# Kernel tuning notes

Measured on AMD Instinct MI355X. Metric: run time of the kernel, lower is better.

## Reference

```python
import jax, jax.numpy as jnp
from jax import lax
import numpy as np

NE = 8          # ne_num
IDX_REF = 4     # ne_num // 2
EPS_BN = 1e-5


def conv2d(x, w, b=None, pad=0):
    out = lax.conv_general_dilated(x, w, (1, 1), [(pad, pad), (pad, pad)],
                                   dimension_numbers=('NCHW', 'OIHW', 'NCHW'))
    if b is not None:
        out = out + b[None, :, None, None]
    return out


def bn(x, gamma, beta):
    # training-mode batch norm (biased variance), as nn.BatchNorm2d in train()
    mu = x.mean(axis=(0, 2, 3), keepdims=True)
    var = x.var(axis=(0, 2, 3), keepdims=True)
    xn = (x - mu) * lax.rsqrt(var + EPS_BN)
    return xn * gamma[None, :, None, None] + beta[None, :, None, None]


def gauss_win(sigma):
    # sigma: (B,1). window_size=3 -> bias = [-1, 0, -1]; pop center of 3x3 -> (B,8)
    bias = jnp.array([-1.0, 0.0, -1.0], dtype=sigma.dtype)
    g = jnp.exp(bias[None, :] / (2.0 * sigma ** 2))            # (B,3)
    w1 = g / g.sum(axis=1, keepdims=True)                      # (B,3)
    w2 = (w1[:, :, None] * w1[:, None, :]).reshape(-1, 9)      # (B,9)
    return jnp.concatenate([w2[:, :4], w2[:, 5:]], axis=1)     # (B,8) center removed


def bilinear(img, y, x):
    # img: (B,H,W); y,x: (B,K,H,W) float sample coords; zero padding outside
    B, H, W = img.shape
    y0 = jnp.floor(y); x0 = jnp.floor(x)
    wy1 = y - y0; wy0 = 1.0 - wy1
    wx1 = x - x0; wx0 = 1.0 - wx1
    imgf = img.reshape(B, -1)

    def gather(yi, xi):
        yii = yi.astype(jnp.int32); xii = xi.astype(jnp.int32)
        valid = (yii >= 0) & (yii < H) & (xii >= 0) & (xii < W)
        idx = jnp.clip(yii, 0, H - 1) * W + jnp.clip(xii, 0, W - 1)
        v = jnp.take_along_axis(imgf, idx.reshape(B, -1), axis=1).reshape(idx.shape)
        return jnp.where(valid, v, 0.0)

    return (wy0 * wx0 * gather(y0, x0) + wy0 * wx1 * gather(y0, x0 + 1.0)
            + wy1 * wx0 * gather(y0 + 1.0, x0) + wy1 * wx1 * gather(y0 + 1.0, x0 + 1.0))


def modulated_deform_conv_1x9(fusion, offset, mask):
    # ModulatedDeformConvFunction with weight=ones(1,1,3,3), bias=0, stride=1,
    # pad=1, dilation=1, groups=1, deformable_groups=1.
    # fusion: (B,1,H,W); offset: (B,9,2,H,W) [per-neighbor (dy,dx)]; mask: (B,9,H,W)
    B, _, H, W = fusion.shape
    k = jnp.arange(9)
    py = (k // 3 - 1).astype(fusion.dtype)[None, :, None, None]
    px = (k % 3 - 1).astype(fusion.dtype)[None, :, None, None]
    hh = jnp.arange(H, dtype=fusion.dtype)[None, None, :, None]
    ww = jnp.arange(W, dtype=fusion.dtype)[None, None, None, :]
    y = hh + py + offset[:, :, 0]
    x = ww + px + offset[:, :, 1]
    samp = bilinear(fusion[:, 0], y, x)            # (B,9,H,W)
    return (mask * samp).sum(axis=1, keepdims=True)  # (B,1,H,W)


def _forward(feat, g1_w, g1_g, g1_b, g2_w, g2_g, g2_b, g3_w, g3_bias,
             f1_w, f1_g, f1_b, f2_w, f2_bias,
             s1_w, s1_b, s2_w, s2_b, s3_w, s3_b,
             oa1_w, oa1_g, oa1_b, oa2_w, oa2_g, oa2_b, oa3_w, oa3_bias,
             aff_scale):
    B, _, H, W = feat.shape
    # guid branch (5x5 convs)
    guid = jax.nn.relu(bn(conv2d(feat, g1_w, pad=2), g1_g, g1_b))
    guid = jax.nn.relu(bn(conv2d(guid, g2_w, pad=2), g2_g, g2_b))
    guid = conv2d(guid, g3_w, g3_bias, pad=2)                      # (B,8,H,W)
    # fuse branch
    f = jax.nn.relu(bn(conv2d(feat, f1_w, pad=1), f1_g, f1_b))
    fusion = jnp.tanh(conv2d(f, f2_w, f2_bias, pad=1))             # (B,1,H,W)
    # sigma branch (CAM, detached input)
    fd = lax.stop_gradient(feat)
    p = fd.mean(axis=(2, 3))                                       # (B,32)
    h = jax.nn.celu(p @ s1_w.T + s1_b)
    h = jax.nn.celu(h @ s2_w.T + s2_b)
    sigma = jax.nn.relu(h @ s3_w.T + s3_b) + 0.001                 # (B,1)
    # get_off_aff(guid, sigma, sigma_gamma=0.2, window_size=3)
    oa = jax.nn.relu(bn(conv2d(guid, oa1_w, pad=2), oa1_g, oa1_b))
    oa = jax.nn.relu(bn(conv2d(oa, oa2_w, pad=2), oa2_g, oa2_b))
    oa = conv2d(oa, oa3_w, oa3_bias, pad=2)                        # (B,24,H,W)
    o1, o2, affc = jnp.split(oa, 3, axis=1)                        # each (B,8,H,W)
    off = jnp.concatenate([o1, o2], axis=1).reshape(B, NE, 2, H, W)
    zero_ref = jnp.zeros((B, 1, 2, H, W), dtype=off.dtype)
    offset = jnp.concatenate([off[:, :IDX_REF], zero_ref, off[:, IDX_REF:]], axis=1)  # (B,9,2,H,W)
    gk = gauss_win(sigma + 0.2)                                    # (B,8)
    aff = jnp.tanh(affc) / (aff_scale + 1e-5) + gk[:, :, None, None]
    sa = jnp.abs(aff).sum(axis=1, keepdims=True) + 1e-5
    sa = jnp.maximum(sa, 1.0)
    aff = aff / sa
    aff_ref = 1.0 - aff.sum(axis=1, keepdims=True)
    aff9 = jnp.concatenate([aff[:, :IDX_REF], aff_ref, aff[:, IDX_REF:]], axis=1)  # (B,9,H,W)
    # gauss_filter (times=1) + abs
    gfusion = jnp.abs(modulated_deform_conv_1x9(fusion, offset, aff9))
    return gfusion


def setup_inputs() -> dict:
    key = jax.random.key(0)
    ks = list(jax.random.split(key, 32))
    B, C, H, W = 8, 32, 320, 320
    ne = NE
    d = {}
    d['feat'] = jax.random.normal(ks[0], (B, C, H, W), jnp.float32)

    def wconv(k, o, i, s):
        return jax.random.normal(k, (o, i, s, s), jnp.float32) * (1.0 / np.sqrt(i * s * s))

    def wlin(k, o, i):
        return jax.random.normal(k, (o, i), jnp.float32) * (1.0 / np.sqrt(i))

    # guid: 32->32 (5), 32->8 (5), 8->8 (5, bias)
    d['g1_w'] = wconv(ks[1], C, C, 5); d['g1_g'] = jnp.ones(C) + 0.1 * jax.random.normal(ks[2], (C,)); d['g1_b'] = 0.1 * jax.random.normal(ks[3], (C,))
    d['g2_w'] = wconv(ks[4], ne, C, 5); d['g2_g'] = jnp.ones(ne) + 0.1 * jax.random.normal(ks[5], (ne,)); d['g2_b'] = 0.1 * jax.random.normal(ks[6], (ne,))
    d['g3_w'] = wconv(ks[7], ne, ne, 5); d['g3_bias'] = 0.1 * jax.random.normal(ks[8], (ne,))
    # fuse: 32->32 (3), 32->1 (3, bias)
    d['f1_w'] = wconv(ks[9], C, C, 3); d['f1_g'] = jnp.ones(C) + 0.1 * jax.random.normal(ks[10], (C,)); d['f1_b'] = 0.1 * jax.random.normal(ks[11], (C,))
    d['f2_w'] = wconv(ks[12], 1, C, 3); d['f2_bias'] = 0.1 * jax.random.normal(ks[13], (1,))
    # gen_sigma CAM: 32->16->16->1
    d['s1_w'] = wlin(ks[14], 16, C); d['s1_b'] = 0.1 * jax.random.normal(ks[15], (16,))
    d['s2_w'] = wlin(ks[16], 16, 16); d['s2_b'] = 0.1 * jax.random.normal(ks[17], (16,))
    d['s3_w'] = wlin(ks[18], 1, 16); d['s3_b'] = 0.1 * jax.random.normal(ks[19], (1,))
    # conv_off_aff: 8->8 (5), 8->24 (5), 24->24 (5, bias)
    d['oa1_w'] = wconv(ks[20], ne, ne, 5); d['oa1_g'] = jnp.ones(ne) + 0.1 * jax.random.normal(ks[21], (ne,)); d['oa1_b'] = 0.1 * jax.random.normal(ks[22], (ne,))
    d['oa2_w'] = wconv(ks[23], 3 * ne, ne, 5); d['oa2_g'] = jnp.ones(3 * ne) + 0.1 * jax.random.normal(ks[24], (3 * ne,)); d['oa2_b'] = 0.1 * jax.random.normal(ks[25], (3 * ne,))
    d['oa3_w'] = wconv(ks[26], 3 * ne, 3 * ne, 5); d['oa3_bias'] = 0.1 * jax.random.normal(ks[27], (3 * ne,))
    # aff_scale_const = aff_gamma * ne_num = 0.5 * 8
    d['aff_scale'] = jnp.full((1,), 4.0, jnp.float32)
    return d


def reference(feat, g1_w, g1_g, g1_b, g2_w, g2_g, g2_b, g3_w, g3_bias,
              f1_w, f1_g, f1_b, f2_w, f2_bias,
              s1_w, s1_b, s2_w, s2_b, s3_w, s3_b,
              oa1_w, oa1_g, oa1_b, oa2_w, oa2_g, oa2_b, oa3_w, oa3_bias,
              aff_scale):
    return _forward(feat, g1_w, g1_g, g1_b, g2_w, g2_g, g2_b, g3_w, g3_bias,
                    f1_w, f1_g, f1_b, f2_w, f2_bias,
                    s1_w, s1_b, s2_w, s2_b, s3_w, s3_b,
                    oa1_w, oa1_g, oa1_b, oa2_w, oa2_g, oa2_b, oa3_w, oa3_bias,
                    aff_scale)
```

## Files before the change

kernel.cpp:

```cpp
#include <hip/hip_runtime.h>
#include <hip/hip_bf16.h>
#include <math.h>

#define B_   8
#define H_   320
#define W_   320
#define HW_  (320*320)

typedef __attribute__((ext_vector_type(8))) short bf16x8;
typedef __attribute__((ext_vector_type(4))) short bf16x4s;
typedef __attribute__((ext_vector_type(4))) float f32x4;

__device__ __forceinline__ short f2b(float v){
    __hip_bfloat16 h = __float2bfloat16(v);
    return *(short*)&h;
}
__device__ __forceinline__ float bf2f(short v){
    unsigned u = ((unsigned)(unsigned short)v) << 16;
    return __uint_as_float(u);
}

__global__ void convert_k(const float* __restrict__ in, short* __restrict__ out,
                          float* __restrict__ psum){
    const int b  = blockIdx.y;
    const int px = blockIdx.x*256 + threadIdx.x;
    const float* src = in + (long)b*32*HW_ + px;
    short* dst = out + ((long)b*HW_ + px)*32;
    float f[32];
    short v[32];
    #pragma unroll
    for (int c=0;c<32;++c){ f[c] = src[(long)c*HW_]; v[c] = f2b(f[c]); }
    #pragma unroll
    for (int s=0;s<4;++s)
        *(bf16x8*)(dst + s*8) = *(bf16x8*)(v + s*8);
    #pragma unroll
    for (int c=0;c<32;++c){
        float s = f[c];
        #pragma unroll
        for (int o=1;o<64;o<<=1) s += __shfl_xor(s, o, 64);
        f[c] = s;
    }
    __shared__ float red[4][32];
    const int lane = threadIdx.x & 63, wid = threadIdx.x >> 6;
    if (lane < 32) red[wid][lane] = f[lane];
    __syncthreads();
    if (threadIdx.x < 32)
        atomicAdd(&psum[b*32 + threadIdx.x],
                  red[0][threadIdx.x]+red[1][threadIdx.x]+red[2][threadIdx.x]+red[3][threadIdx.x]);
}

__global__ void repack_k(const float* __restrict__ sf1, const float* __restrict__ sf2,
                         const float* __restrict__ sg1, const float* __restrict__ sg2,
                         const float* __restrict__ sg3, const float* __restrict__ so1,
                         const float* __restrict__ so2, const float* __restrict__ so3,
                         short* __restrict__ dst){
    const int cum[8]  = {9216,13824,39424,52224,55808,59392,66560,92160};
    const int CINs[8] = {32,32,32,32, 8, 8, 8,24};
    const int CIps[8] = {32,32,32,32, 8, 8, 8,32};
    const int COUTs[8]= {32, 1,32, 8, 8, 8,24,24};
    const int MTs[8]  = { 2, 1, 2, 1, 1, 1, 2, 2};
    const int Ks[8]   = { 3, 3, 5, 5, 5, 5, 5, 5};
    int i = blockIdx.x*256 + threadIdx.x;
    if (i >= 92160) return;
    int s = 0;
    while (i >= cum[s]) ++s;
    const int base = s ? cum[s-1] : 0;
    const int il = i - base;
    const float* src = (s==0)?sf1:(s==1)?sf2:(s==2)?sg1:(s==3)?sg2:(s==4)?sg3:(s==5)?so1:(s==6)?so2:so3;
    const int kl   = il & 31;
    const int co_l = (il >> 5) & 15;
    const int rem  = il >> 9;
    const int MT = MTs[s];
    const int mt = rem % MT;
    const int c  = rem / MT;
    const int K = Ks[s];
    int tap, ci;
    if (CIps[s] == 32){ tap = (c % K)*K + (c / K); ci = kl; }
    else              { tap = c*4 + (kl>>3); ci = kl & 7; }
    const int co = mt*16 + co_l;
    float v = 0.f;
    if (co < COUTs[s] && ci < CINs[s] && tap < K*K){
        const int ky = tap / K, kx = tap - ky*K;
        v = src[((co*CINs[s] + ci)*K + ky)*K + kx];
    }
    dst[i] = f2b(v);
}

__device__ __forceinline__
float deform_px(const float* val, const float* __restrict__ fus_b,
                const float* __restrict__ gk_b, float inv_s, int y, int x){
    float aff[8]; float sa = 0.f;
    #pragma unroll
    for (int n=0;n<8;++n){
        float a = tanhf(val[16+n]) * inv_s + gk_b[n];
        aff[n] = a; sa += fabsf(a);
    }
    sa += 1e-5f;
    sa = fmaxf(sa, 1.f);
    const float isa = 1.f/sa;
    float ssum = 0.f;
    #pragma unroll
    for (int n=0;n<8;++n){ aff[n] *= isa; ssum += aff[n]; }
    const float aff_ref = 1.f - ssum;

    float o = 0.f;
    #pragma unroll
    for (int k=0;k<9;++k){
        float dy, dx, m;
        if (k == 4){ dy = 0.f; dx = 0.f; m = aff_ref; }
        else {
            const int n = (k < 4) ? k : k-1;
            dy = val[2*n];
            dx = val[2*n+1];
            m  = aff[n];
        }
        float yy = (float)(y + k/3 - 1) + dy;
        float xx = (float)(x + k%3 - 1) + dx;
        float y0f = floorf(yy), x0f = floorf(xx);
        int   y0 = (int)y0f,    x0i = (int)x0f;
        float wy1 = yy - y0f, wy0 = 1.f - wy1;
        float wx1 = xx - x0f, wx0 = 1.f - wx1;
        float v00 = (y0  >=0 && y0  <H_ && x0i  >=0 && x0i  <W_) ? fus_b[ y0   *W_ + x0i  ] : 0.f;
        float v01 = (y0  >=0 && y0  <H_ && x0i+1>=0 && x0i+1<W_) ? fus_b[ y0   *W_ + x0i+1] : 0.f;
        float v10 = (y0+1>=0 && y0+1<H_ && x0i  >=0 && x0i  <W_) ? fus_b[(y0+1)*W_ + x0i  ] : 0.f;
        float v11 = (y0+1>=0 && y0+1<H_ && x0i+1>=0 && x0i+1<W_) ? fus_b[(y0+1)*W_ + x0i+1] : 0.f;
        o += m * (wy0*(wx0*v00 + wx1*v01) + wy1*(wx0*v10 + wx1*v11));
    }
    return fabsf(o);
}

template<int CIN, int CIp, int COUT, int MT, int K,
         bool IN_BN, bool OUT_STATS, int OUT_MODE, int OCP>
__global__ __launch_bounds__(256, 4)
void mconv_k(const void* __restrict__ inv,
             const float* __restrict__ bn_sum, const float* __restrict__ bn_sq,
             const float* __restrict__ gamma, const float* __restrict__ beta,
             const short* __restrict__ wr, const float* __restrict__ bias,
             void* __restrict__ outv,
             float* __restrict__ osum, float* __restrict__ osq,
             const float* __restrict__ fus, const float* __restrict__ gk,
             const float* __restrict__ aff_scale){
    constexpr int PAD = K/2;
    constexpr int TH  = 8;
    constexpr int LW  = 32 + K - 1;
    constexpr int LH  = TH + K - 1;
    constexpr int STR = (CIp==32) ? 40 : 8;
    constexpr int NTAPS  = K*K;
    constexpr int NCHUNK = (CIp==32) ? NTAPS : (NTAPS*CIp + 31)/32;
    constexpr int INB  = LH*LW*STR*2;
    constexpr int DUMPB = 256*33*4;
    constexpr int LDSB = (OUT_MODE==3 && INB < DUMPB) ? DUMPB : INB;

    __shared__ __align__(16) char ldsraw[LDSB];
    short* lds_in = (short*)ldsraw;
    __shared__ float sc_sh[2][32];
    __shared__ float red[2][4][32];

    const int tid = threadIdx.x;
    const int b   = blockIdx.z;
    const int x0  = blockIdx.x*32, y0 = blockIdx.y*TH;

    if (IN_BN){
        if (tid < 32){
            float s = 1.f, sh2 = 0.f;
            if (tid < CIN){
                const float invN = 1.f/(float)(B_*HW_);
                float mu  = bn_sum[tid]*invN;
                float var = bn_sq[tid]*invN - mu*mu;
                s   = gamma[tid] * rsqrtf(var + 1e-5f);
                sh2 = beta[tid] - mu*s;
            }
            sc_sh[0][tid] = s;
            sc_sh[1][tid] = sh2;
        }
        __syncthreads();
    }

    {
        const short* src = (const short*)inv + (long)b*HW_*CIp;
        constexpr int SEGS = CIp/8;
        constexpr int NU = LH*LW*SEGS;
        constexpr int NIT = (NU + 255)/256;
        bf16x8 vv[NIT];
        int    la[NIT];
        bool   ib[NIT];
        #pragma unroll
        for (int it=0; it<NIT; ++it){
            const int u = tid + it*256;
            bf16x8 v = {0,0,0,0,0,0,0,0};
            bool inb = false;
            int addr = 0;
            if (u < NU){
                const int r   = u / (LW*SEGS);
                const int rem = u - r*(LW*SEGS);
                const int xl  = rem / SEGS;
                const int seg = rem - xl*SEGS;
                const int gy = y0 + r - PAD, gx = x0 + xl - PAD;
                addr = (r*LW + xl)*STR + seg*8;
                inb = (gy>=0 && gy<H_ && gx>=0 && gx<W_);
                if (inb)
                    v = *(const bf16x8*)(src + ((long)gy*W_ + gx)*CIp + seg*8);
            }
            vv[it] = v; la[it] = addr; ib[it] = inb;
        }
        #pragma unroll
        for (int it=0; it<NIT; ++it){
            const int u = tid + it*256;
            if (u < NU){
                bf16x8 v = vv[it];
                if (IN_BN && ib[it]){
                    const int seg = (u - (u/SEGS)*SEGS);
                    #pragma unroll
                    for (int j=0;j<8;++j){
                        float f = bf2f(v[j]);
                        f = fmaxf(fmaf(f, sc_sh[0][seg*8+j], sc_sh[1][seg*8+j]), 0.f);
                        v[j] = f2b(f);
                    }
                }
                *(bf16x8*)&lds_in[la[it]] = v;
            }
        }
    }
    __syncthreads();

    const int lane = tid & 63;
    const int wv   = tid >> 6;
    const int pxn  = lane & 15;
    const int quad = lane >> 4;
    const int row0 = 2*wv;

    const f32x4 zero = {0.f, 0.f, 0.f, 0.f};
    f32x4 acc[2][MT][2];
    #pragma unroll
    for (int rr=0;rr<2;++rr)
        #pragma unroll
        for (int m=0;m<MT;++m){ acc[rr][m][0] = zero; acc[rr][m][1] = zero; }

    if constexpr (CIp == 32){
        const short* bbase = lds_in + (row0*LW + pxn)*STR + quad*8;
        bf16x8 aA[4][MT];
        #pragma unroll
        for (int v=0; v<3; ++v){
            if (v < NTAPS){
                #pragma unroll
                for (int m=0;m<MT;++m)
                    aA[v][m] = *(const bf16x8*)(wr + ((v*MT + m)*16 + pxn)*32 + quad*8);
            }
        }
        #pragma unroll
        for (int kx=0; kx<K; ++kx){
            bf16x8 b0[2], b1[2], b2[2];
            #pragma unroll
            for (int n=0;n<2;++n){
                b0[n] = *(const bf16x8*)(bbase + (0*LW + kx + n*16)*STR);
                b1[n] = *(const bf16x8*)(bbase + (1*LW + kx + n*16)*STR);
            }
            #pragma unroll
            for (int ky=0; ky<K; ++ky){
                const int v = kx*K + ky;
                if (v+3 < NTAPS){
                    #pragma unroll
                    for (int m=0;m<MT;++m)
                        aA[(v+3)&3][m] = *(const bf16x8*)(wr + (((v+3)*MT + m)*16 + pxn)*32 + quad*8);
                }
                if (ky < K-1){
                    #pragma unroll
                    for (int n=0;n<2;++n)
                        b2[n] = *(const bf16x8*)(bbase + ((ky+2)*LW + kx + n*16)*STR);
                }
                #pragma unroll
                for (int m=0;m<MT;++m){
                    acc[0][m][0] = __builtin_amdgcn_mfma_f32_16x16x32_bf16(aA[v&3][m], b0[0], acc[0][m][0], 0,0,0);
                    acc[0][m][1] = __builtin_amdgcn_mfma_f32_16x16x32_bf16(aA[v&3][m], b0[1], acc[0][m][1], 0,0,0);
                    acc[1][m][0] = __builtin_amdgcn_mfma_f32_16x16x32_bf16(aA[v&3][m], b1[0], acc[1][m][0], 0,0,0);
                    acc[1][m][1] = __builtin_amdgcn_mfma_f32_16x16x32_bf16(aA[v&3][m], b1[1], acc[1][m][1], 0,0,0);
                }
                if (ky < K-1){
                    #pragma unroll
                    for (int n=0;n<2;++n){ b0[n] = b1[n]; b1[n] = b2[n]; }
                }
            }
        }
    } else {
        auto bptr = [&](int c, int rr)->const short*{
            const int row = row0 + rr;
            int t = c*4 + quad;
            if (t >= NTAPS) t = 0;
            const int ky = t / K, kx = t - ky*K;
            return lds_in + ((row+ky)*LW + kx + pxn)*STR;
        };

        bf16x8 acur[MT], anxt[MT];
        #pragma unroll
        for (int m=0;m<MT;++m)
            acur[m] = *(const bf16x8*)(wr + ((m*16 + pxn)*32 + quad*8));
        bf16x8 bc[2][2];
        #pragma unroll
        for (int rr=0;rr<2;++rr){
            const short* bp = bptr(0, rr);
            bc[rr][0] = *(const bf16x8*)bp;
            bc[rr][1] = *(const bf16x8*)(bp + 16*STR);
        }

        #pragma unroll
        for (int c=0; c<NCHUNK; ++c){
            bf16x8 bnx[2][2];
            #pragma unroll
            for (int rr=0;rr<2;++rr){ bnx[rr][0] = bc[rr][0]; bnx[rr][1] = bc[rr][1]; }
            if (c+1 < NCHUNK){
                #pragma unroll
                for (int m=0;m<MT;++m)
                    anxt[m] = *(const bf16x8*)(wr + ((((c+1)*MT + m)*16 + pxn)*32 + quad*8));
                #pragma unroll
                for (int rr=0;rr<2;++rr){
                    const short* bpn = bptr(c+1, rr);
                    bnx[rr][0] = *(const bf16x8*)bpn;
                    bnx[rr][1] = *(const bf16x8*)(bpn + 16*STR);
                }
            }
            #pragma unroll
            for (int m=0;m<MT;++m)
                #pragma unroll
                for (int rr=0;rr<2;++rr){
                    acc[rr][m][0] = __builtin_amdgcn_mfma_f32_16x16x32_bf16(acur[m], bc[rr][0], acc[rr][m][0], 0,0,0);
                    acc[rr][m][1] = __builtin_amdgcn_mfma_f32_16x16x32_bf16(acur[m], bc[rr][1], acc[rr][m][1], 0,0,0);
                }
            #pragma unroll
            for (int m=0;m<MT;++m) acur[m] = anxt[m];
            #pragma unroll
            for (int rr=0;rr<2;++rr){ bc[rr][0] = bnx[rr][0]; bc[rr][1] = bnx[rr][1]; }
        }
    }

    if (OUT_STATS){
        #pragma unroll
        for (int m=0;m<MT;++m){
            #pragma unroll
            for (int r=0;r<4;++r){
                float v  = acc[0][m][0][r] + acc[0][m][1][r]
                         + acc[1][m][0][r] + acc[1][m][1][r];
                float v2 = acc[0][m][0][r]*acc[0][m][0][r] + acc[0][m][1][r]*acc[0][m][1][r]
                         + acc[1][m][0][r]*acc[1][m][0][r] + acc[1][m][1][r]*acc[1][m][1][r];
                #pragma unroll
                for (int o=1;o<16;o<<=1){
                    v  += __shfl_xor(v,  o, 64);
                    v2 += __shfl_xor(v2, o, 64);
                }
                if (pxn == 0){
                    red[0][wv][m*16 + quad*4 + r] = v;
                    red[1][wv][m*16 + quad*4 + r] = v2;
                }
            }
        }
        __syncthreads();
        if (tid < MT*16 && tid < COUT){
            atomicAdd(&osum[tid], red[0][0][tid]+red[0][1][tid]+red[0][2][tid]+red[0][3][tid]);
            atomicAdd(&osq[tid],  red[1][0][tid]+red[1][1][tid]+red[1][2][tid]+red[1][3][tid]);
        }
    }

    if (OUT_MODE == 3){
        float* out = (float*)outv;
        __syncthreads();
        float* dumpf = (float*)ldsraw;
        #pragma unroll
        for (int rr=0;rr<2;++rr){
            const int row = row0 + rr;
            #pragma unroll
            for (int m=0;m<MT;++m)
                #pragma unroll
                for (int n=0;n<2;++n)
                    #pragma unroll
                    for (int r=0;r<4;++r)
                        dumpf[(row*32 + n*16 + pxn)*33 + (m*16 + quad*4 + r)] = acc[rr][m][n][r];
        }
        __syncthreads();
        {
            float val[24];
            #pragma unroll
            for (int c2=0;c2<24;++c2) val[c2] = dumpf[tid*33 + c2] + bias[c2];
            const int yy = y0 + (tid>>5), xx = x0 + (tid&31);
            const float inv_s = 1.f/(aff_scale[0] + 1e-5f);
            out[(long)b*HW_ + yy*W_ + xx] =
                deform_px(val, fus + (long)b*HW_, gk + b*8, inv_s, yy, xx);
        }
    } else if (OUT_MODE == 2){
        float* out = (float*)outv;
        #pragma unroll
        for (int rr=0;rr<2;++rr){
            const int y = y0 + row0 + rr;
            #pragma unroll
            for (int m=0;m<MT;++m){
                #pragma unroll
                for (int r=0;r<4;++r){
                    const int co = m*16 + quad*4 + r;
                    if (co < COUT){
                        float* op = out + (((long)b*COUT + co)*H_ + y)*W_ + x0;
                        #pragma unroll
                        for (int n=0;n<2;++n)
                            op[n*16 + pxn] = tanhf(acc[rr][m][n][r] + bias[co]);
                    }
                }
            }
        }
    } else {
        short* o = (short*)outv;
        #pragma unroll
        for (int rr=0;rr<2;++rr){
            const int y = y0 + row0 + rr;
            #pragma unroll
            for (int m=0;m<MT;++m){
                const int co0 = m*16 + quad*4;
                if (co0 < OCP){
                    #pragma unroll
                    for (int n=0;n<2;++n){
                        bf16x4s pk;
                        #pragma unroll
                        for (int r=0;r<4;++r){
                            float f = acc[rr][m][n][r];
                            if (OUT_MODE == 1) f += bias[co0+r];
                            pk[r] = f2b(f);
                        }
                        const long px = ((long)b*H_ + y)*W_ + x0 + n*16 + pxn;
                        *(bf16x4s*)(o + px*OCP + co0) = pk;
                    }
                }
            }
        }
    }
}

__global__ void sigma_k(const float* __restrict__ p,
                        const float* s1w, const float* s1b,
                        const float* s2w, const float* s2b,
                        const float* s3w, const float* s3b,
                        float* __restrict__ gk){
    const int b = threadIdx.x;
    if (b >= B_) return;
    float pb[32];
    for (int j=0;j<32;++j) pb[j] = p[b*32+j] * (1.f/(float)HW_);
    float h1[16], h2[16];
    for (int i=0;i<16;++i){
        float t = s1b[i];
        for (int j=0;j<32;++j) t = fmaf(pb[j], s1w[i*32+j], t);
        h1[i] = t > 0.f ? t : expm1f(t);
    }
    for (int i=0;i<16;++i){
        float t = s2b[i];
        for (int j=0;j<16;++j) t = fmaf(h1[j], s2w[i*16+j], t);
        h2[i] = t > 0.f ? t : expm1f(t);
    }
    float t = s3b[0];
    for (int j=0;j<16;++j) t = fmaf(h2[j], s3w[j], t);
    float sigma = fmaxf(t, 0.f) + 0.001f;
    float sg = sigma + 0.2f;
    float e = expf(-1.f/(2.f*sg*sg));
    float inv = 1.f/(2.f*e + 1.f);
    float a = e*inv, c = inv;
    float* g = gk + b*8;
    g[0]=a*a; g[1]=a*c; g[2]=a*a; g[3]=c*a; g[4]=c*a; g[5]=a*a; g[6]=a*c; g[7]=a*a;
}

extern "C" void kernel_launch(void* const* d_in, const int* in_sizes, int n_in,
                              void* d_out, int out_size, void* d_ws, size_t ws_size,
                              hipStream_t stream){
    const float* feat    = (const float*)d_in[0];
    const float* g1_w    = (const float*)d_in[1];
    const float* g1_g    = (const float*)d_in[2];
    const float* g1_b    = (const float*)d_in[3];
    const float* g2_w    = (const float*)d_in[4];
    const float* g2_g    = (const float*)d_in[5];
    const float* g2_b    = (const float*)d_in[6];
    const float* g3_w    = (const float*)d_in[7];
    const float* g3_bias = (const float*)d_in[8];
    const float* f1_w    = (const float*)d_in[9];
    const float* f1_g    = (const float*)d_in[10];
    const float* f1_b    = (const float*)d_in[11];
    const float* f2_w    = (const float*)d_in[12];
    const float* f2_bias = (const float*)d_in[13];
    const float* s1w     = (const float*)d_in[14];
    const float* s1b     = (const float*)d_in[15];
    const float* s2w     = (const float*)d_in[16];
    const float* s2b     = (const float*)d_in[17];
    const float* s3w     = (const float*)d_in[18];
    const float* s3b     = (const float*)d_in[19];
    const float* oa1_w   = (const float*)d_in[20];
    const float* oa1_g   = (const float*)d_in[21];
    const float* oa1_b   = (const float*)d_in[22];
    const float* oa2_w   = (const float*)d_in[23];
    const float* oa2_g   = (const float*)d_in[24];
    const float* oa2_b   = (const float*)d_in[25];
    const float* oa3_w   = (const float*)d_in[26];
    const float* oa3_bias= (const float*)d_in[27];
    const float* aff_scale=(const float*)d_in[28];
    float* out = (float*)d_out;

    char* ws = (char*)d_ws;
    short* FEAT = (short*)(ws + 0L);
    short* A1   = (short*)(ws + 52428800L);
    short* A2   = (short*)(ws + 104857600L);
    short* GUID = (short*)(ws + 117964800L);
    float* FUS  = (float*)(ws + 131072000L);
    float* SM   = (float*)(ws + 134348800L);
    short* OA2  = A1;

    float* sum = SM;
    float* sq  = SM + 320;
    float* p   = SM + 640;
    float* gk  = SM + 896;
    short* WBs = (short*)(SM + 960);
    short* w_f1 = WBs + 0;
    short* w_f2 = WBs + 9216;
    short* w_g1 = WBs + 13824;
    short* w_g2 = WBs + 39424;
    short* w_g3 = WBs + 52224;
    short* w_o1 = WBs + 55808;
    short* w_o2 = WBs + 59392;
    short* w_o3 = WBs + 66560;

    hipMemsetAsync(sum, 0, 896*sizeof(float), stream);

    repack_k<<<dim3(360), dim3(256), 0, stream>>>(
        f1_w, f2_w, g1_w, g2_w, g3_w, oa1_w, oa2_w, oa3_w, WBs);
    convert_k<<<dim3(HW_/256, B_), dim3(256), 0, stream>>>(feat, FEAT, p);

    sigma_k<<<dim3(1), dim3(64), 0, stream>>>(p, s1w, s1b, s2w, s2b, s3w, s3b, gk);

    const dim3 cgrid(10, 40, 8), cblk(256);
    #define MCONV(CIN,CIp,COUT,MT,K,IBN,OST,OM,OCP) \
        mconv_k<CIN,CIp,COUT,MT,K,IBN,OST,OM,OCP><<<cgrid,cblk,0,stream>>>

    MCONV(32,32,32,2,3,false,true ,0,32)(FEAT, nullptr, nullptr, nullptr, nullptr,
        w_f1, nullptr, A1, sum+0*64, sq+0*64, nullptr, nullptr, nullptr);
    MCONV(32,32, 1,1,3,true ,false,2, 0)(A1, sum+0*64, sq+0*64, f1_g, f1_b,
        w_f2, f2_bias, FUS, nullptr, nullptr, nullptr, nullptr, nullptr);

    MCONV(32,32,32,2,5,false,true ,0,32)(FEAT, nullptr, nullptr, nullptr, nullptr,
        w_g1, nullptr, A1, sum+1*64, sq+1*64, nullptr, nullptr, nullptr);
    MCONV(32,32, 8,1,5,true ,true ,0, 8)(A1, sum+1*64, sq+1*64, g1_g, g1_b,
        w_g2, nullptr, A2, sum+2*64, sq+2*64, nullptr, nullptr, nullptr);
    MCONV( 8, 8, 8,1,5,true ,false,1, 8)(A2, sum+2*64, sq+2*64, g2_g, g2_b,
        w_g3, g3_bias, GUID, nullptr, nullptr, nullptr, nullptr, nullptr);

    MCONV( 8, 8, 8,1,5,false,true ,0, 8)(GUID, nullptr, nullptr, nullptr, nullptr,
        w_o1, nullptr, A2, sum+3*64, sq+3*64, nullptr, nullptr, nullptr);
    MCONV( 8, 8,24,2,5,true ,true ,0,32)(A2, sum+3*64, sq+3*64, oa1_g, oa1_b,
        w_o2, nullptr, OA2, sum+4*64, sq+4*64, nullptr, nullptr, nullptr);
    MCONV(24,32,24,2,5,true ,false,3, 0)(OA2, sum+4*64, sq+4*64, oa2_g, oa2_b,
        w_o3, oa3_bias, out, nullptr, nullptr, FUS, gk, aff_scale);
    #undef MCONV
}
```

Measured before the change: 672.0 us.

## Preload conv weights before tile staging and pin load/MFMA order with sched barriers

Weight fragments are now loaded from global memory before the input halo is staged into LDS. For CIp==8 all chunks are preloaded; for CIp==32 one kx column is held while the next column is prefetched. Scheduling barriers keep these loads ahead of the MFMA groups so global latency overlaps with LDS staging and compute. This raises VGPR pressure considerably (all chunks or two K×MT weight sets live at once), which may reduce occupancy or cause spills for large K/MT.

```diff
diff --git a/kernel.cpp b/kernel.cpp
--- a/kernel.cpp
+++ b/kernel.cpp
@@ -160,6 +160,12 @@
     const int b   = blockIdx.z;
     const int x0  = blockIdx.x*32, y0 = blockIdx.y*TH;
 
+    const int lane = tid & 63;
+    const int wv   = tid >> 6;
+    const int pxn  = lane & 15;
+    const int quad = lane >> 4;
+    const int row0 = 2*wv;
+
     if (IN_BN){
         if (tid < 32){
             float s = 1.f, sh2 = 0.f;
@@ -174,6 +180,24 @@
             sc_sh[1][tid] = sh2;
         }
         __syncthreads();
+    }
+
+    constexpr int KC = (CIp==32) ? K : 1;
+    bf16x8 aC[KC][MT];
+    bf16x8 aAll[(CIp==8)?NCHUNK:1][MT];
+
+    if constexpr (CIp == 32){
+        #pragma unroll
+        for (int ky=0; ky<K; ++ky)
+            #pragma unroll
+            for (int m=0;m<MT;++m)
+                aC[ky][m] = *(const bf16x8*)(wr + ((ky*MT + m)*16 + pxn)*32 + quad*8);
+    } else {
+        #pragma unroll
+        for (int c=0;c<NCHUNK;++c)
+            #pragma unroll
+            for (int m=0;m<MT;++m)
+                aAll[c][m] = *(const bf16x8*)(wr + (((c*MT + m)*16 + pxn)*32 + quad*8));
     }
 
     {
@@ -203,6 +227,7 @@
             }
             vv[it] = v; la[it] = addr; ib[it] = inb;
         }
+        __builtin_amdgcn_sched_barrier(0);
         #pragma unroll
         for (int it=0; it<NIT; ++it){
             const int u = tid + it*256;
@@ -223,12 +248,6 @@
     }
     __syncthreads();
 
-    const int lane = tid & 63;
-    const int wv   = tid >> 6;
-    const int pxn  = lane & 15;
-    const int quad = lane >> 4;
-    const int row0 = 2*wv;
-
     const f32x4 zero = {0.f, 0.f, 0.f, 0.f};
     f32x4 acc[2][MT][2];
     #pragma unroll
@@ -238,15 +257,7 @@
 
     if constexpr (CIp == 32){
         const short* bbase = lds_in + (row0*LW + pxn)*STR + quad*8;
-        bf16x8 aA[4][MT];
-        #pragma unroll
-        for (int v=0; v<3; ++v){
-            if (v < NTAPS){
-                #pragma unroll
-                for (int m=0;m<MT;++m)
-                    aA[v][m] = *(const bf16x8*)(wr + ((v*MT + m)*16 + pxn)*32 + quad*8);
-            }
-        }
+        bf16x8 aN[K][MT];
         #pragma unroll
         for (int kx=0; kx<K; ++kx){
             bf16x8 b0[2], b1[2], b2[2];
@@ -257,28 +268,35 @@
             }
             #pragma unroll
             for (int ky=0; ky<K; ++ky){
-                const int v = kx*K + ky;
-                if (v+3 < NTAPS){
+                if (kx+1 < K){
+                    const int vn = (kx+1)*K + ky;
                     #pragma unroll
                     for (int m=0;m<MT;++m)
-                        aA[(v+3)&3][m] = *(const bf16x8*)(wr + (((v+3)*MT + m)*16 + pxn)*32 + quad*8);
+                        aN[ky][m] = *(const bf16x8*)(wr + ((vn*MT + m)*16 + pxn)*32 + quad*8);
                 }
                 if (ky < K-1){
                     #pragma unroll
                     for (int n=0;n<2;++n)
                         b2[n] = *(const bf16x8*)(bbase + ((ky+2)*LW + kx + n*16)*STR);
                 }
+                __builtin_amdgcn_sched_barrier(0);
                 #pragma unroll
                 for (int m=0;m<MT;++m){
-                    acc[0][m][0] = __builtin_amdgcn_mfma_f32_16x16x32_bf16(aA[v&3][m], b0[0], acc[0][m][0], 0,0,0);
-                    acc[0][m][1] = __builtin_amdgcn_mfma_f32_16x16x32_bf16(aA[v&3][m], b0[1], acc[0][m][1], 0,0,0);
-                    acc[1][m][0] = __builtin_amdgcn_mfma_f32_16x16x32_bf16(aA[v&3][m], b1[0], acc[1][m][0], 0,0,0);
-                    acc[1][m][1] = __builtin_amdgcn_mfma_f32_16x16x32_bf16(aA[v&3][m], b1[1], acc[1][m][1], 0,0,0);
+                    acc[0][m][0] = __builtin_amdgcn_mfma_f32_16x16x32_bf16(aC[ky][m], b0[0], acc[0][m][0], 0,0,0);
+                    acc[0][m][1] = __builtin_amdgcn_mfma_f32_16x16x32_bf16(aC[ky][m], b0[1], acc[0][m][1], 0,0,0);
+                    acc[1][m][0] = __builtin_amdgcn_mfma_f32_16x16x32_bf16(aC[ky][m], b1[0], acc[1][m][0], 0,0,0);
+                    acc[1][m][1] = __builtin_amdgcn_mfma_f32_16x16x32_bf16(aC[ky][m], b1[1], acc[1][m][1], 0,0,0);
                 }
                 if (ky < K-1){
                     #pragma unroll
                     for (int n=0;n<2;++n){ b0[n] = b1[n]; b1[n] = b2[n]; }
                 }
+            }
+            if (kx+1 < K){
+                #pragma unroll
+                for (int ky=0; ky<K; ++ky)
+                    #pragma unroll
+                    for (int m=0;m<MT;++m) aC[ky][m] = aN[ky][m];
             }
         }
     } else {
@@ -290,10 +308,6 @@
             return lds_in + ((row+ky)*LW + kx + pxn)*STR;
         };
 
-        bf16x8 acur[MT], anxt[MT];
-        #pragma unroll
-        for (int m=0;m<MT;++m)
-            acur[m] = *(const bf16x8*)(wr + ((m*16 + pxn)*32 + quad*8));
         bf16x8 bc[2][2];
         #pragma unroll
         for (int rr=0;rr<2;++rr){
@@ -309,24 +323,20 @@
             for (int rr=0;rr<2;++rr){ bnx[rr][0] = bc[rr][0]; bnx[rr][1] = bc[rr][1]; }
             if (c+1 < NCHUNK){
                 #pragma unroll
-                for (int m=0;m<MT;++m)
-                    anxt[m] = *(const bf16x8*)(wr + ((((c+1)*MT + m)*16 + pxn)*32 + quad*8));
-                #pragma unroll
                 for (int rr=0;rr<2;++rr){
                     const short* bpn = bptr(c+1, rr);
                     bnx[rr][0] = *(const bf16x8*)bpn;
                     bnx[rr][1] = *(const bf16x8*)(bpn + 16*STR);
                 }
             }
+            __builtin_amdgcn_sched_barrier(0);
             #pragma unroll
             for (int m=0;m<MT;++m)
                 #pragma unroll
                 for (int rr=0;rr<2;++rr){
-                    acc[rr][m][0] = __builtin_amdgcn_mfma_f32_16x16x32_bf16(acur[m], bc[rr][0], acc[rr][m][0], 0,0,0);
-                    acc[rr][m][1] = __builtin_amdgcn_mfma_f32_16x16x32_bf16(acur[m], bc[rr][1], acc[rr][m][1], 0,0,0);
-                }
-            #pragma unroll
-            for (int m=0;m<MT;++m) acur[m] = anxt[m];
+                    acc[rr][m][0] = __builtin_amdgcn_mfma_f32_16x16x32_bf16(aAll[c][m], bc[rr][0], acc[rr][m][0], 0,0,0);
+                    acc[rr][m][1] = __builtin_amdgcn_mfma_f32_16x16x32_bf16(aAll[c][m], bc[rr][1], acc[rr][m][1], 0,0,0);
+                }
             #pragma unroll
             for (int rr=0;rr<2;++rr){ bc[rr][0] = bnx[rr][0]; bc[rr][1] = bnx[rr][1]; }
         }
```

Result: faster. 598.9 us (-10.9%).
